# Performance work log

Hardware: AMD Instinct MI355X
Metric: run time of the kernel (lower is better)

The kernel has to match this reference:

```python
import jax, jax.numpy as jnp
import numpy as np

EMB = 1024
HEADS = 16
HEAD_SIZE = EMB // HEADS


def setup_inputs() -> dict:
    key = jax.random.key(0)
    ks = jax.random.split(key, 10)
    B, L = 2, 2048
    s = 1.0 / np.sqrt(EMB)
    inp = {
        "x": jax.random.normal(ks[0], (B, L, EMB), jnp.float32),
        "ln_g": jnp.ones((EMB,), jnp.float32),
        "ln_b": jnp.zeros((EMB,), jnp.float32),
        "Wq": jax.random.normal(ks[1], (EMB, EMB), jnp.float32) * s,
        "bq": jnp.zeros((EMB,), jnp.float32),
        "Wk": jax.random.normal(ks[2], (EMB, EMB), jnp.float32) * s,
        "bk": jnp.zeros((EMB,), jnp.float32),
        "Wv": jax.random.normal(ks[3], (EMB, EMB), jnp.float32) * s,
        "bv": jnp.zeros((EMB,), jnp.float32),
        "Wo": jax.random.normal(ks[4], (EMB, EMB), jnp.float32) * s,
        "bo": jnp.zeros((EMB,), jnp.float32),
    }
    return inp


def _attn_block(x, ln_g, ln_b, Wq, bq, Wk, bk, Wv, bv, Wo, bo):
    B, L, D = x.shape
    # LayerNorm (eps=1e-5 as torch default)
    mu = jnp.mean(x, axis=-1, keepdims=True)
    var = jnp.mean(jnp.square(x - mu), axis=-1, keepdims=True)
    h = (x - mu) * jax.lax.rsqrt(var + 1e-5) * ln_g + ln_b
    # QKV projections (torch Linear: x @ W.T + b), split heads -> [B,H,L,hs]
    def heads(y):
        return y.reshape(B, L, HEADS, HEAD_SIZE).transpose(0, 2, 1, 3)
    q = heads(h @ Wq.T + bq)
    k = heads(h @ Wk.T + bk)
    v = heads(h @ Wv.T + bv)
    # scaled dot-product attention (no mask; dropout = identity in eval)
    scores = jnp.einsum("bhqd,bhkd->bhqk", q, k) * (HEAD_SIZE ** -0.5)
    w = jax.nn.softmax(scores, axis=-1)
    o = jnp.einsum("bhqk,bhkd->bhqd", w, v)
    o = o.transpose(0, 2, 1, 3).reshape(B, L, D)
    return o @ Wo.T + bo


def reference(x, ln_g, ln_b, Wq, bq, Wk, bk, Wv, bv, Wo, bo):
    return _attn_block(x, ln_g, ln_b, Wq, bq, Wk, bk, Wv, bv, Wo, bo)
```

## Files before the change

kernel.cpp:

```cpp
#include <hip/hip_runtime.h>
#include <stdint.h>

#define EMB 1024
#define SEQL 2048
#define HEADS 16
#define HS 64

typedef __attribute__((ext_vector_type(8))) short bfx8;
typedef __attribute__((ext_vector_type(4))) float f32x4;
typedef __attribute__((ext_vector_type(16))) float f32x16;
typedef __attribute__((ext_vector_type(4))) unsigned short us4;
typedef __attribute__((ext_vector_type(8))) unsigned short us8;

__device__ __forceinline__ unsigned short f2bf(float f) {
  union { float f; unsigned u; } x; x.f = f;
  unsigned r = x.u + 0x7fffu + ((x.u >> 16) & 1u);
  return (unsigned short)(r >> 16);
}

__device__ __forceinline__ unsigned cvtpk(float lo, float hi) {
  unsigned r;
  asm("v_cvt_pk_bf16_f32 %0, %1, %2" : "=v"(r) : "v"(lo), "v"(hi));
  return r;
}

__device__ __forceinline__ float expv(float x) {
  float r;
  asm("v_exp_f32 %0, %1" : "=v"(r) : "v"(x));
  return r;
}

__device__ __forceinline__ float max3f(float a, float b, float c) {
  float r;
  asm("v_max3_f32 %0, %1, %2, %3" : "=v"(r) : "v"(a), "v"(b), "v"(c));
  return r;
}

__device__ __forceinline__ void gll16(const void* g, void* l) {
  __builtin_amdgcn_global_load_lds(
      (const __attribute__((address_space(1))) unsigned int*)g,
      (__attribute__((address_space(3))) unsigned int*)l, 16, 0, 0);
}

__global__ __launch_bounds__(256) void lncvt_kernel(
    const float* __restrict__ x, const float* __restrict__ gam,
    const float* __restrict__ bet, unsigned short* __restrict__ h,
    const float* __restrict__ s0, const float* __restrict__ s1,
    const float* __restrict__ s2, const float* __restrict__ s3,
    unsigned short* __restrict__ d) {
  const int tid = threadIdx.x;
  if (blockIdx.x < 4096) {
    const int row = blockIdx.x;
    const float4 v = reinterpret_cast<const float4*>(x + (size_t)row * EMB)[tid];
    float s = v.x + v.y + v.z + v.w;
    float sq = v.x * v.x + v.y * v.y + v.z * v.z + v.w * v.w;
    #pragma unroll
    for (int m = 1; m < 64; m <<= 1) {
      s += __shfl_xor(s, m, 64);
      sq += __shfl_xor(sq, m, 64);
    }
    __shared__ float red[8];
    const int lane = tid & 63, wave = tid >> 6;
    if (lane == 0) { red[wave] = s; red[wave + 4] = sq; }
    __syncthreads();
    s = red[0] + red[1] + red[2] + red[3];
    sq = red[4] + red[5] + red[6] + red[7];
    const float mu = s * (1.0f / EMB);
    const float var = sq * (1.0f / EMB) - mu * mu;
    const float rs = rsqrtf(var + 1e-5f);
    const float4 gg = reinterpret_cast<const float4*>(gam)[tid];
    const float4 bb = reinterpret_cast<const float4*>(bet)[tid];
    us4 o;
    o.x = f2bf((v.x - mu) * rs * gg.x + bb.x);
    o.y = f2bf((v.y - mu) * rs * gg.y + bb.y);
    o.z = f2bf((v.z - mu) * rs * gg.z + bb.z);
    o.w = f2bf((v.w - mu) * rs * gg.w + bb.w);
    reinterpret_cast<us4*>(h + (size_t)row * EMB)[tid] = o;
  } else {
    const int bid = blockIdx.x - 4096;
    const int m = bid >> 10;
    const int blk = bid & 1023;
    const float* s = (m == 0) ? s0 : (m == 1) ? s1 : (m == 2) ? s2 : s3;
    unsigned short* dd = d + (size_t)m * EMB * EMB;
    const int idx = blk * 256 + tid;
    const float4 v = reinterpret_cast<const float4*>(s)[idx];
    us4 o;
    o.x = f2bf(v.x); o.y = f2bf(v.y); o.z = f2bf(v.z); o.w = f2bf(v.w);
    reinterpret_cast<us4*>(dd)[idx] = o;
  }
}

__device__ __forceinline__ void gemm_tile(
    const unsigned short* __restrict__ Ag, const unsigned short* __restrict__ Bg,
    int m0, int n0, int K, char* lA, char* lB, f32x4 acc[4][4]) {
  const int tid = threadIdx.x;
  const int lane = tid & 63, wave = tid >> 6;
  const int g = lane >> 4, c = lane & 15;
  const int wr = wave >> 1, wc = wave & 1;

  const f32x4 zero = {0.f, 0.f, 0.f, 0.f};
  #pragma unroll
  for (int i = 0; i < 4; ++i)
    #pragma unroll
    for (int j = 0; j < 4; ++j) acc[i][j] = zero;

  const int Dbase = (wave * 4 * 64 + lane) * 16;
  for (int k0 = 0; k0 < K; k0 += 64) {
    __syncthreads();
    #pragma unroll
    for (int i = 0; i < 4; ++i) {
      const int Db = Dbase + i * 1024;
      const int row = Db >> 7;
      const int col = ((Db & 127) ^ ((row & 7) << 4)) >> 1;
      gll16(Ag + (size_t)(m0 + row) * K + (k0 + col), lA + (wave * 4 + i) * 1024);
      gll16(Bg + (size_t)(n0 + row) * K + (k0 + col), lB + (wave * 4 + i) * 1024);
    }
    __syncthreads();
    #pragma unroll
    for (int kf = 0; kf < 2; ++kf) {
      bfx8 af[4], bfr[4];
      #pragma unroll
      for (int i = 0; i < 4; ++i) {
        const int ra = wr * 64 + i * 16 + c;
        af[i] = *(const bfx8*)(lA + ra * 128 + ((kf * 64 + g * 16) ^ ((ra & 7) << 4)));
        const int rb = wc * 64 + i * 16 + c;
        bfr[i] = *(const bfx8*)(lB + rb * 128 + ((kf * 64 + g * 16) ^ ((rb & 7) << 4)));
      }
      #pragma unroll
      for (int i = 0; i < 4; ++i)
        #pragma unroll
        for (int j = 0; j < 4; ++j)
          acc[i][j] = __builtin_amdgcn_mfma_f32_16x16x32_bf16(af[i], bfr[j], acc[i][j], 0, 0, 0);
    }
  }
}

__global__ __launch_bounds__(256, 3) void qkv_gemm(
    const unsigned short* __restrict__ h, const unsigned short* __restrict__ wbf,
    const float* __restrict__ bq, const float* __restrict__ bk,
    const float* __restrict__ bv, unsigned short* __restrict__ qb,
    unsigned short* __restrict__ kb, unsigned short* __restrict__ vtb) {
  __shared__ char lA[16384];
  __shared__ char lB[16384];
  f32x4 acc[4][4];
  const int m0 = blockIdx.x * 128;
  const int n0g = blockIdx.y * 128;
  const int mat = n0g >> 10;
  const int n0 = n0g & 1023;
  gemm_tile(h, wbf + (size_t)mat * EMB * EMB, m0, n0, EMB, lA, lB, acc);

  const float* bias = (mat == 0) ? bq : (mat == 1) ? bk : bv;
  const int tid = threadIdx.x;
  const int lane = tid & 63, wave = tid >> 6;
  const int g = lane >> 4, c = lane & 15;
  const int wr = wave >> 1, wc = wave & 1;

  if (mat < 2) {
    #pragma unroll
    for (int i = 0; i < 4; ++i) {
      #pragma unroll
      for (int j = 0; j < 4; ++j) {
        const int col = n0 + wc * 64 + j * 16 + c;
        const float bz = bias[col];
        const int hh = col >> 6, d = col & 63;
        #pragma unroll
        for (int r = 0; r < 4; ++r) {
          const int row = m0 + wr * 64 + i * 16 + 4 * g + r;
          const int bidx = row >> 11, l = row & 2047;
          const unsigned short bv16 = f2bf(acc[i][j][r] + bz);
          unsigned short* dst = (mat == 0) ? qb : kb;
          dst[(((size_t)(bidx * HEADS + hh) * SEQL + l) << 6) + d] = bv16;
        }
      }
    }
  } else {
    __syncthreads();
    char* wbase = (wc ? lB : lA);
    #pragma unroll
    for (int i = 0; i < 4; ++i) {
      #pragma unroll
      for (int j = 0; j < 4; ++j) {
        const int colL = wc * 64 + j * 16 + c;
        const float bz = bias[n0 + colL];
        uint2 w;
        w.x = cvtpk(acc[i][j][0] + bz, acc[i][j][1] + bz);
        w.y = cvtpk(acc[i][j][2] + bz, acc[i][j][3] + bz);
        const int off = (wr * 128 + i * 32 + 8 * g) ^ ((colL & 7) << 4);
        *reinterpret_cast<uint2*>(wbase + (colL & 63) * 256 + off) = w;
      }
    }
    __syncthreads();
    const char* rbase = (wave >= 2) ? lB : lA;
    const int colbase = ((wave >= 2) ? 64 : 0) + (wave & 1) * 32;
    const int g0 = lane & 15;
    const int bidx = m0 >> 11;
    const int l0 = (m0 & 2047) + g0 * 8;
    #pragma unroll
    for (int dc = 0; dc < 8; ++dc) {
      const int colL = colbase + dc * 4 + (lane >> 4);
      const int slot = g0 ^ (colL & 7);
      const us8 v = *reinterpret_cast<const us8*>(
          rbase + (colL & 63) * 256 + slot * 16);
      const int colG = n0 + colL;
      const int hh = colG >> 6, d = colG & 63;
      *reinterpret_cast<us8*>(
          vtb + ((size_t)(bidx * HEADS + hh) * HS + d) * SEQL + l0) = v;
    }
  }
}

__global__ __launch_bounds__(256, 2) void attn_kernel(
    const unsigned short* __restrict__ qb, const unsigned short* __restrict__ kb,
    const unsigned short* __restrict__ vtb, unsigned short* __restrict__ ob) {
  __shared__ char lK[4][8192];
  __shared__ char lV[4][8192];
  const int tid = threadIdx.x, lane = tid & 63, wave = tid >> 6;
  const int l31 = lane & 31, hi = lane >> 5;
  const int sw = (l31 & 7) << 4;
  const int qblk = blockIdx.x;
  const int bh = blockIdx.y;
  const unsigned short* qp = qb + (size_t)bh * SEQL * HS;
  const unsigned short* kp = kb + (size_t)bh * SEQL * HS;
  const unsigned short* vp = vtb + (size_t)bh * HS * SEQL;
  const int qbase = qblk * 128 + wave * 32;

  bfx8 aq[4];
  #pragma unroll
  for (int kf = 0; kf < 4; ++kf)
    aq[kf] = *(const bfx8*)(qp + (size_t)(qbase + l31) * HS + kf * 16 + hi * 8);

  const float SCL = 0.125f * 1.44269504089f;
  const float THR = 11.5416f;
  const bfx8 vone = {0x3F80, 0x3F80, 0x3F80, 0x3F80, 0x3F80, 0x3F80, 0x3F80, 0x3F80};

  float mst = -INFINITY;
  f32x16 oacc0, oacc1, lacc;
  const f32x16 zero16 = {0.f,0.f,0.f,0.f,0.f,0.f,0.f,0.f,0.f,0.f,0.f,0.f,0.f,0.f,0.f,0.f};
  oacc0 = zero16; oacc1 = zero16; lacc = zero16;

  const int sbase = wave * 2048;
  const int Db0 = sbase + lane * 16, Db1 = Db0 + 1024;
  const int sr0 = Db0 >> 7, sr1 = Db1 >> 7;
  const int sc0 = ((Db0 & 127) ^ ((sr0 & 7) << 4)) >> 1;
  const int sc1 = ((Db1 & 127) ^ ((sr1 & 7) << 4)) >> 1;
  const unsigned short* k0s = kp + (size_t)sr0 * HS + sc0;
  const unsigned short* k1s = kp + (size_t)sr1 * HS + sc1;
  const unsigned short* v0s = vp + (size_t)sr0 * SEQL + sc0;
  const unsigned short* v1s = vp + (size_t)sr1 * SEQL + sc1;

  gll16(k0s, lK[0] + sbase); gll16(k1s, lK[0] + sbase + 1024);
  gll16(v0s, lV[0] + sbase); gll16(v1s, lV[0] + sbase + 1024);
  gll16(k0s + 64 * HS, lK[1] + sbase); gll16(k1s + 64 * HS, lK[1] + sbase + 1024);
  gll16(v0s + 64, lV[1] + sbase); gll16(v1s + 64, lV[1] + sbase + 1024);

  const unsigned short* kf0 = k0s + 2 * 64 * HS;
  const unsigned short* kf1 = k1s + 2 * 64 * HS;
  const unsigned short* vf0 = v0s + 2 * 64;
  const unsigned short* vf1 = v1s + 2 * 64;

  auto proc_half = [&](const char* kptr, const char* lVc, const int kfv) {
    f32x16 s;
    __builtin_amdgcn_s_setprio(1);
    {
      const bfx8 a0 = *(const bfx8*)(kptr + l31 * 128 + ((16 * hi) ^ sw));
      s = __builtin_amdgcn_mfma_f32_32x32x16_bf16(a0, aq[0], zero16, 0, 0, 0);
    }
    #pragma unroll
    for (int kf = 1; kf < 4; ++kf) {
      const int ko = (32 * kf + 16 * hi) ^ sw;
      const bfx8 a0 = *(const bfx8*)(kptr + l31 * 128 + ko);
      s = __builtin_amdgcn_mfma_f32_32x32x16_bf16(a0, aq[kf], s, 0, 0, 0);
    }
    __builtin_amdgcn_s_setprio(0);

    bfx8 vb0, vb1, vb2, vb3;
    {
      const int vo0 = (32 * kfv + 16 * hi) ^ sw;
      const int vo1 = (32 * (kfv + 1) + 16 * hi) ^ sw;
      vb0 = *(const bfx8*)(lVc + l31 * 128 + vo0);
      vb1 = *(const bfx8*)(lVc + l31 * 128 + 4096 + vo0);
      vb2 = *(const bfx8*)(lVc + l31 * 128 + vo1);
      vb3 = *(const bfx8*)(lVc + l31 * 128 + 4096 + vo1);
    }

    float m0 = max3f(s[0], s[1], s[2]);
    float m1 = max3f(s[3], s[4], s[5]);
    float m2 = max3f(s[6], s[7], s[8]);
    float m3 = max3f(s[9], s[10], s[11]);
    float m4 = max3f(s[12], s[13], s[14]);
    m0 = max3f(m0, m1, m2);
    m3 = max3f(m3, m4, s[15]);
    const float sm = fmaxf(m0, m3);

    if (__any(sm * SCL > mst + THR)) {
      float mt = sm * SCL;
      mt = fmaxf(mt, __shfl_xor(mt, 32, 64));
      const float mn = fmaxf(mst, mt);
      const float al = exp2f(mst - mn);
      mst = mn;
      #pragma unroll
      for (int r = 0; r < 16; ++r) {
        const int qi = (r & 3) + 8 * (r >> 2) + 4 * hi;
        const float alq = __shfl(al, qi, 64);
        lacc[r] *= alq;
        oacc0[r] *= alq;
        oacc1[r] *= alq;
      }
    }

    #pragma unroll
    for (int r = 0; r < 16; ++r) s[r] = expv(fmaf(s[r], SCL, -mst));

    __builtin_amdgcn_s_setprio(1);
    #pragma unroll
    for (int h2 = 0; h2 < 2; ++h2) {
      const int bb = 8 * h2;
      unsigned w0 = cvtpk(s[bb + 0], s[bb + 1]), w2 = cvtpk(s[bb + 4], s[bb + 5]);
      unsigned w1 = cvtpk(s[bb + 2], s[bb + 3]), w3 = cvtpk(s[bb + 6], s[bb + 7]);
      asm("v_permlane32_swap_b32 %0, %1" : "+v"(w0), "+v"(w2));
      asm("v_permlane32_swap_b32 %0, %1" : "+v"(w1), "+v"(w3));
      union { unsigned u[4]; bfx8 v; } pa;
      pa.u[0] = w0; pa.u[1] = w1; pa.u[2] = w2; pa.u[3] = w3;
      lacc = __builtin_amdgcn_mfma_f32_32x32x16_bf16(pa.v, vone, lacc, 0, 0, 0);
      const bfx8 b0 = h2 ? vb2 : vb0;
      const bfx8 b1 = h2 ? vb3 : vb1;
      oacc0 = __builtin_amdgcn_mfma_f32_32x32x16_bf16(pa.v, b0, oacc0, 0, 0, 0);
      oacc1 = __builtin_amdgcn_mfma_f32_32x32x16_bf16(pa.v, b1, oacc1, 0, 0, 0);
    }
    __builtin_amdgcn_s_setprio(0);
  };

  auto step = [&](const char* lKc, const char* lVc, char* nK, char* nV,
                  const int wait, const bool doStage) {
    if (doStage) {
      gll16(kf0, nK + sbase); gll16(kf1, nK + sbase + 1024);
      gll16(vf0, nV + sbase); gll16(vf1, nV + sbase + 1024);
      kf0 += 64 * HS; kf1 += 64 * HS; vf0 += 64; vf1 += 64;
    }
    if (wait == 8)      asm volatile("s_waitcnt vmcnt(8)" ::: "memory");
    else if (wait == 4) asm volatile("s_waitcnt vmcnt(4)" ::: "memory");
    else                asm volatile("s_waitcnt vmcnt(0)" ::: "memory");
    __builtin_amdgcn_s_barrier();
    __builtin_amdgcn_sched_barrier(0);
    proc_half(lKc,        lVc, 0);
    proc_half(lKc + 4096, lVc, 2);
  };

  for (int t = 0; t < 28; t += 4) {
    step(lK[0], lV[0], lK[2], lV[2], 8, true);
    step(lK[1], lV[1], lK[3], lV[3], 8, true);
    step(lK[2], lV[2], lK[0], lV[0], 8, true);
    step(lK[3], lV[3], lK[1], lV[1], 8, true);
  }
  step(lK[0], lV[0], lK[2], lV[2], 8, true);
  step(lK[1], lV[1], lK[3], lV[3], 8, true);
  step(lK[2], lV[2], lK[0], lV[0], 4, false);
  step(lK[3], lV[3], lK[1], lV[1], 0, false);

  const int b = bh >> 4, hh = bh & 15;
  #pragma unroll
  for (int r = 0; r < 16; ++r) {
    const float inv = 1.f / lacc[r];
    const int row = qbase + (r & 3) + 8 * (r >> 2) + 4 * hi;
    unsigned short* orow = ob + (size_t)(b * SEQL + row) * EMB + hh * 64;
    orow[l31] = f2bf(oacc0[r] * inv);
    orow[32 + l31] = f2bf(oacc1[r] * inv);
  }
}

__global__ __launch_bounds__(256, 2) void out_gemm(
    const unsigned short* __restrict__ ob, const unsigned short* __restrict__ wo,
    const float* __restrict__ bo, float* __restrict__ out) {
  __shared__ char lA[16384];
  __shared__ char lB[16384];
  f32x4 acc[4][4];
  const int m0 = blockIdx.x * 128;
  const int n0 = blockIdx.y * 128;
  gemm_tile(ob, wo, m0, n0, EMB, lA, lB, acc);

  const int lane = threadIdx.x & 63, wave = threadIdx.x >> 6;
  const int g = lane >> 4, c = lane & 15;
  const int wr = wave >> 1, wc = wave & 1;
  #pragma unroll
  for (int i = 0; i < 4; ++i)
    #pragma unroll
    for (int j = 0; j < 4; ++j) {
      const int col = n0 + wc * 64 + j * 16 + c;
      const float bz = bo[col];
      #pragma unroll
      for (int r = 0; r < 4; ++r) {
        const int row = m0 + wr * 64 + i * 16 + 4 * g + r;
        out[(size_t)row * EMB + col] = acc[i][j][r] + bz;
      }
    }
}

extern "C" void kernel_launch(void* const* d_in, const int* in_sizes, int n_in,
                              void* d_out, int out_size, void* d_ws, size_t ws_size,
                              hipStream_t stream) {
  const float* x   = (const float*)d_in[0];
  const float* lng = (const float*)d_in[1];
  const float* lnb = (const float*)d_in[2];
  const float* Wq  = (const float*)d_in[3];
  const float* bq  = (const float*)d_in[4];
  const float* Wk  = (const float*)d_in[5];
  const float* bk  = (const float*)d_in[6];
  const float* Wv  = (const float*)d_in[7];
  const float* bv  = (const float*)d_in[8];
  const float* Wo  = (const float*)d_in[9];
  const float* bo  = (const float*)d_in[10];

  char* ws = (char*)d_ws;
  unsigned short* h   = (unsigned short*)(ws);
  unsigned short* wbf = (unsigned short*)(ws + 8388608);
  unsigned short* qb  = (unsigned short*)(ws + 16777216);
  unsigned short* kb  = (unsigned short*)(ws + 25165824);
  unsigned short* vtb = (unsigned short*)(ws + 33554432);
  unsigned short* ob  = (unsigned short*)(ws + 41943040);
  float* out = (float*)d_out;

  lncvt_kernel<<<dim3(8192), dim3(256), 0, stream>>>(x, lng, lnb, h,
                                                     Wq, Wk, Wv, Wo, wbf);
  qkv_gemm<<<dim3(32, 24), dim3(256), 0, stream>>>(h, wbf, bq, bk, bv, qb, kb, vtb);
  attn_kernel<<<dim3(16, 32), dim3(256), 0, stream>>>(qb, kb, vtb, ob);
  out_gemm<<<dim3(32, 8), dim3(256), 0, stream>>>(ob, wbf + (size_t)3 * EMB * EMB, bo, out);
}
```

Measured before the change: 117.2 us.

## Software-pipeline QK and softmax-PV across tiles in attention; halve out_gemm N tile

The attention loop now computes the QK scores for the next K tile before running softmax and PV on the previous tile's scores, so the matrix-core work and the exp/max work of adjacent tiles can overlap. The barrier and wait now come before staging the next global loads, and the running max starts at 0 instead of -inf. The output projection switches to a 128x64 tile with a new GEMM helper, doubling the grid to 512 blocks to fill more compute units. The pipelining adds register pressure from keeping two score tiles live and changes buffer-reuse timing, which risks races and spills.

```diff
diff --git a/kernel.cpp b/kernel.cpp
--- a/kernel.cpp
+++ b/kernel.cpp
@@ -135,6 +135,61 @@
   }
 }
 
+__device__ __forceinline__ void gemm_tile_n64(
+    const unsigned short* __restrict__ Ag, const unsigned short* __restrict__ Bg,
+    int m0, int n0, int K, char* lA, char* lB, f32x4 acc[4][2]) {
+  const int tid = threadIdx.x;
+  const int lane = tid & 63, wave = tid >> 6;
+  const int g = lane >> 4, c = lane & 15;
+  const int wr = wave >> 1, wc = wave & 1;
+
+  const f32x4 zero = {0.f, 0.f, 0.f, 0.f};
+  #pragma unroll
+  for (int i = 0; i < 4; ++i)
+    #pragma unroll
+    for (int j = 0; j < 2; ++j) acc[i][j] = zero;
+
+  const int DbaseA = (wave * 4 * 64 + lane) * 16;
+  const int DbaseB = (wave * 2 * 64 + lane) * 16;
+  for (int k0 = 0; k0 < K; k0 += 64) {
+    __syncthreads();
+    #pragma unroll
+    for (int i = 0; i < 4; ++i) {
+      const int Db = DbaseA + i * 1024;
+      const int row = Db >> 7;
+      const int col = ((Db & 127) ^ ((row & 7) << 4)) >> 1;
+      gll16(Ag + (size_t)(m0 + row) * K + (k0 + col), lA + (wave * 4 + i) * 1024);
+    }
+    #pragma unroll
+    for (int i = 0; i < 2; ++i) {
+      const int Db = DbaseB + i * 1024;
+      const int row = Db >> 7;
+      const int col = ((Db & 127) ^ ((row & 7) << 4)) >> 1;
+      gll16(Bg + (size_t)(n0 + row) * K + (k0 + col), lB + (wave * 2 + i) * 1024);
+    }
+    __syncthreads();
+    #pragma unroll
+    for (int kf = 0; kf < 2; ++kf) {
+      bfx8 af[4], bfr[2];
+      #pragma unroll
+      for (int i = 0; i < 4; ++i) {
+        const int ra = wr * 64 + i * 16 + c;
+        af[i] = *(const bfx8*)(lA + ra * 128 + ((kf * 64 + g * 16) ^ ((ra & 7) << 4)));
+      }
+      #pragma unroll
+      for (int j = 0; j < 2; ++j) {
+        const int rb = wc * 32 + j * 16 + c;
+        bfr[j] = *(const bfx8*)(lB + rb * 128 + ((kf * 64 + g * 16) ^ ((rb & 7) << 4)));
+      }
+      #pragma unroll
+      for (int i = 0; i < 4; ++i)
+        #pragma unroll
+        for (int j = 0; j < 2; ++j)
+          acc[i][j] = __builtin_amdgcn_mfma_f32_16x16x32_bf16(af[i], bfr[j], acc[i][j], 0, 0, 0);
+    }
+  }
+}
+
 __global__ __launch_bounds__(256, 3) void qkv_gemm(
     const unsigned short* __restrict__ h, const unsigned short* __restrict__ wbf,
     const float* __restrict__ bq, const float* __restrict__ bk,
@@ -233,10 +288,12 @@
   const float THR = 11.5416f;
   const bfx8 vone = {0x3F80, 0x3F80, 0x3F80, 0x3F80, 0x3F80, 0x3F80, 0x3F80, 0x3F80};
 
-  float mst = -INFINITY;
+  float mst = 0.0f;
   f32x16 oacc0, oacc1, lacc;
+  f32x16 spa, spb;
   const f32x16 zero16 = {0.f,0.f,0.f,0.f,0.f,0.f,0.f,0.f,0.f,0.f,0.f,0.f,0.f,0.f,0.f,0.f};
   oacc0 = zero16; oacc1 = zero16; lacc = zero16;
+  spa = zero16; spb = zero16;
 
   const int sbase = wave * 2048;
   const int Db0 = sbase + lane * 16, Db1 = Db0 + 1024;
@@ -258,9 +315,8 @@
   const unsigned short* vf0 = v0s + 2 * 64;
   const unsigned short* vf1 = v1s + 2 * 64;
 
-  auto proc_half = [&](const char* kptr, const char* lVc, const int kfv) {
+  auto qk_half = [&](const char* kptr) -> f32x16 {
     f32x16 s;
-    __builtin_amdgcn_s_setprio(1);
     {
       const bfx8 a0 = *(const bfx8*)(kptr + l31 * 128 + ((16 * hi) ^ sw));
       s = __builtin_amdgcn_mfma_f32_32x32x16_bf16(a0, aq[0], zero16, 0, 0, 0);
@@ -271,8 +327,10 @@
       const bfx8 a0 = *(const bfx8*)(kptr + l31 * 128 + ko);
       s = __builtin_amdgcn_mfma_f32_32x32x16_bf16(a0, aq[kf], s, 0, 0, 0);
     }
-    __builtin_amdgcn_s_setprio(0);
-
+    return s;
+  };
+
+  auto smpv = [&](f32x16& s, const char* lVc, const int kfv) {
     bfx8 vb0, vb1, vb2, vb3;
     {
       const int vo0 = (32 * kfv + 16 * hi) ^ sw;
@@ -330,32 +388,40 @@
     __builtin_amdgcn_s_setprio(0);
   };
 
-  auto step = [&](const char* lKc, const char* lVc, char* nK, char* nV,
-                  const int wait, const bool doStage) {
+  auto step = [&](const char* lKc, const char* lVp, char* nK, char* nV,
+                  const int wait, const bool doStage, const bool doSMPV) {
+    if (wait == 4) asm volatile("s_waitcnt vmcnt(4)" ::: "memory");
+    else           asm volatile("s_waitcnt vmcnt(0)" ::: "memory");
+    __builtin_amdgcn_s_barrier();
+    __builtin_amdgcn_sched_barrier(0);
     if (doStage) {
       gll16(kf0, nK + sbase); gll16(kf1, nK + sbase + 1024);
       gll16(vf0, nV + sbase); gll16(vf1, nV + sbase + 1024);
       kf0 += 64 * HS; kf1 += 64 * HS; vf0 += 64; vf1 += 64;
     }
-    if (wait == 8)      asm volatile("s_waitcnt vmcnt(8)" ::: "memory");
-    else if (wait == 4) asm volatile("s_waitcnt vmcnt(4)" ::: "memory");
-    else                asm volatile("s_waitcnt vmcnt(0)" ::: "memory");
-    __builtin_amdgcn_s_barrier();
-    __builtin_amdgcn_sched_barrier(0);
-    proc_half(lKc,        lVc, 0);
-    proc_half(lKc + 4096, lVc, 2);
+    __builtin_amdgcn_s_setprio(1);
+    f32x16 na = qk_half(lKc);
+    f32x16 nb = qk_half(lKc + 4096);
+    __builtin_amdgcn_s_setprio(0);
+    if (doSMPV) {
+      smpv(spa, lVp, 0);
+      smpv(spb, lVp, 2);
+    }
+    spa = na; spb = nb;
   };
 
-  for (int t = 0; t < 28; t += 4) {
-    step(lK[0], lV[0], lK[2], lV[2], 8, true);
-    step(lK[1], lV[1], lK[3], lV[3], 8, true);
-    step(lK[2], lV[2], lK[0], lV[0], 8, true);
-    step(lK[3], lV[3], lK[1], lV[1], 8, true);
-  }
-  step(lK[0], lV[0], lK[2], lV[2], 8, true);
-  step(lK[1], lV[1], lK[3], lV[3], 8, true);
-  step(lK[2], lV[2], lK[0], lV[0], 4, false);
-  step(lK[3], lV[3], lK[1], lV[1], 0, false);
+  step(lK[0], lV[3], lK[2], lV[2], 4, true, false);
+  for (int g4 = 0; g4 < 7; ++g4) {
+    step(lK[1], lV[0], lK[3], lV[3], 4, true, true);
+    step(lK[2], lV[1], lK[0], lV[0], 4, true, true);
+    step(lK[3], lV[2], lK[1], lV[1], 4, true, true);
+    step(lK[0], lV[3], lK[2], lV[2], 4, true, true);
+  }
+  step(lK[1], lV[0], lK[3], lV[3], 4, true, true);
+  step(lK[2], lV[1], lK[0], lV[0], 4, false, true);
+  step(lK[3], lV[2], lK[0], lV[0], 0, false, true);
+  smpv(spa, lV[3], 0);
+  smpv(spb, lV[3], 2);
 
   const int b = bh >> 4, hh = bh & 15;
   #pragma unroll
@@ -372,11 +438,11 @@
     const unsigned short* __restrict__ ob, const unsigned short* __restrict__ wo,
     const float* __restrict__ bo, float* __restrict__ out) {
   __shared__ char lA[16384];
-  __shared__ char lB[16384];
-  f32x4 acc[4][4];
+  __shared__ char lB[8192];
+  f32x4 acc[4][2];
   const int m0 = blockIdx.x * 128;
-  const int n0 = blockIdx.y * 128;
-  gemm_tile(ob, wo, m0, n0, EMB, lA, lB, acc);
+  const int n0 = blockIdx.y * 64;
+  gemm_tile_n64(ob, wo, m0, n0, EMB, lA, lB, acc);
 
   const int lane = threadIdx.x & 63, wave = threadIdx.x >> 6;
   const int g = lane >> 4, c = lane & 15;
@@ -384,8 +450,8 @@
   #pragma unroll
   for (int i = 0; i < 4; ++i)
     #pragma unroll
-    for (int j = 0; j < 4; ++j) {
-      const int col = n0 + wc * 64 + j * 16 + c;
+    for (int j = 0; j < 2; ++j) {
+      const int col = n0 + wc * 32 + j * 16 + c;
       const float bz = bo[col];
       #pragma unroll
       for (int r = 0; r < 4; ++r) {
@@ -423,5 +489,5 @@
                                                      Wq, Wk, Wv, Wo, wbf);
   qkv_gemm<<<dim3(32, 24), dim3(256), 0, stream>>>(h, wbf, bq, bk, bv, qb, kb, vtb);
   attn_kernel<<<dim3(16, 32), dim3(256), 0, stream>>>(qb, kb, vtb, ob);
-  out_gemm<<<dim3(32, 8), dim3(256), 0, stream>>>(ob, wbf + (size_t)3 * EMB * EMB, bo, out);
-}
+  out_gemm<<<dim3(32, 16), dim3(256), 0, stream>>>(ob, wbf + (size_t)3 * EMB * EMB, bo, out);
+}
```

Result: faster. 112.9 us (-3.7%).
